# Kernel tuning notes

Measured on AMD Instinct MI355X. Metric: run time of the kernel, lower is better.

The kernel has to match this reference:

```python
import jax, jax.numpy as jnp
import numpy as np

N_NEURONS = 50000
N_BKG = 100
N_SYN_BASIS = 5
N_EDGES = 500000
BATCH = 1
SEQ_T = 250
BKG_RATE_PROB = 0.25  # bkg_firing_rate(250) * 0.001


def setup_inputs() -> dict:
    key = jax.random.key(0)
    k_w, k_tau, k_sp, k_r, k_c = jax.random.split(key, 5)
    weights = jax.random.normal(k_w, (N_EDGES,), dtype=jnp.float32)
    tau_syn = jax.random.uniform(k_tau, (N_EDGES, N_SYN_BASIS), dtype=jnp.float32)
    # Bernoulli background spikes, shape [B*T, n_bkg_units]
    spikes = (jax.random.uniform(k_sp, (BATCH * SEQ_T, N_BKG)) < BKG_RATE_PROB).astype(jnp.float32)
    rows = jax.random.randint(k_r, (N_EDGES,), 0, N_NEURONS, dtype=jnp.int32)
    cols = jax.random.randint(k_c, (N_EDGES,), 0, N_BKG, dtype=jnp.int32)
    return {"weights": weights, "tau_syn": tau_syn, "spikes": spikes,
            "rows": rows, "cols": cols}


def reference(weights, tau_syn, spikes, rows, cols):
    # Per-receptor edge values: weights[e] * tau_syn[e, r]  -> [E, R]
    vals = weights[:, None] * tau_syn
    # Densify the (identical-structure) sparse matrix once for all receptors;
    # duplicate (row, col) indices accumulate, matching tf.sparse semantics
    # used through sparse_dense_matmul. W: [N, K, R]
    W = jnp.zeros((N_NEURONS, N_BKG, N_SYN_BASIS), dtype=spikes.dtype).at[rows, cols].add(vals)
    # i_receptor[r] = sparse_w_in @ spikes.T -> stacked [R, N, BT];
    # tf.transpose reverses axes -> [BT, N, R]; fused here as one einsum.
    out = jnp.einsum('nkr,bk->bnr', W, spikes)  # [BT, N, R]
    return out.reshape(BATCH, SEQ_T, N_NEURONS * N_SYN_BASIS)
```

## Files before the change

kernel.cpp:

```cpp
#include <hip/hip_runtime.h>


#define N_NEURONS 50000
#define N_BKG     100
#define N_SYN     5
#define N_EDGES   500000
#define SEQ_T     250
#define NCOL      (N_NEURONS * N_SYN)
#define RPB       16
#define NBINS     (N_NEURONS / RPB)
#define NPART     8
#define CAP_P     64
#define RECS_BIN  (NPART * CAP_P)
#define CPADF     80
#define BCOLS     80
#define STRIDE_J  37

#define LDS_BYTES 32000

#define WS_COUNT_OFF 0
#define WS_SPB_OFF   131072
#define WS_REC_OFF   262144

typedef __attribute__((ext_vector_type(8))) short bf16x8;
typedef __attribute__((ext_vector_type(4))) float f32x4;

__device__ inline unsigned short bf16_rne(float f) {
    unsigned u = __builtin_bit_cast(unsigned, f);
    u += 0x7FFFu + ((u >> 16) & 1u);
    return (unsigned short)(u >> 16);
}
__device__ inline float bf16_up(unsigned hw) {
    return __builtin_bit_cast(float, hw << 16);
}

__global__ __launch_bounds__(256) void bucket_kernel(
        const float* __restrict__ weights,
        const float* __restrict__ tau,
        const int*   __restrict__ rows,
        const int*   __restrict__ cols,
        const float* __restrict__ spikes,
        unsigned* __restrict__ count,
        uint4* __restrict__ rec,
        bf16x8* __restrict__ spbf) {
    int gid = blockIdx.x * 256 + threadIdx.x;
    if (gid < 4096) {
        int lane = gid & 63;
        int kk   = (gid >> 6) & 3;
        int nt   = gid >> 8;
        int t    = nt * 16 + (lane & 15);
        int k0   = kk * 32 + (lane >> 4) * 8;
        bf16x8 v;
#pragma unroll
        for (int i = 0; i < 8; ++i) {
            float s = 0.f;
            if (t < SEQ_T && (k0 + i) < N_BKG)
                s = spikes[t * N_BKG + k0 + i];
            v[i] = (short)bf16_rne(s);
        }
        spbf[gid] = v;
    }
    if (gid >= N_EDGES) return;
    int row = rows[gid];
    int col = cols[gid];
    float w = weights[gid];
    const float* tp = tau + (size_t)gid * N_SYN;
    int bin  = row >> 4;
    int part = blockIdx.x & (NPART - 1);
    unsigned slot = atomicAdd(&count[part * NBINS + bin], 1u);
    if (slot >= CAP_P) return;
    uint4 r;
    r.x = ((unsigned)col << 4) | (unsigned)(row & 15);
    r.y = (unsigned)bf16_rne(w * tp[0]) | ((unsigned)bf16_rne(w * tp[1]) << 16);
    r.z = (unsigned)bf16_rne(w * tp[2]) | ((unsigned)bf16_rne(w * tp[3]) << 16);
    r.w = (unsigned)bf16_rne(w * tp[4]);
    rec[(size_t)bin * RECS_BIN + part * CAP_P + slot] = r;
}

__global__ __launch_bounds__(256, 4) void fused_kernel(
        const unsigned* __restrict__ count,
        const uint4* __restrict__ rec,
        const bf16x8* __restrict__ spbf,
        float* __restrict__ out) {
    __shared__ __align__(16) char lds[LDS_BYTES];
    float* slice = (float*)lds;

    const int tid = threadIdx.x;
    const int l   = tid & 63;
    const int wv  = tid >> 6;
    const int lc  = l & 15;
    const int lq  = l >> 4;

    const int orig = blockIdx.x;
    const int xcd  = orig & 7;
    const int j    = orig >> 3;
    const int qx   = (xcd < 5) ? 391 : 390;
    const int base = (xcd < 5) ? xcd * 391 : 5 * 391 + (xcd - 5) * 390;
    const int bin  = base + (j * STRIDE_J) % qx;

    const uint4* rbin = rec + (size_t)bin * RECS_BIN;
    unsigned cntA = count[wv * NBINS + bin];
    unsigned cntB = count[(4 + wv) * NBINS + bin];
    if (cntA > CAP_P) cntA = CAP_P;
    if (cntB > CAP_P) cntB = CAP_P;
    uint4 ra = rbin[wv * CAP_P + l];
    uint4 rb = rbin[(4 + wv) * CAP_P + l];
    bool havea = (unsigned)l < cntA;
    bool haveb = (unsigned)l < cntB;

    {
        f32x4* s4 = (f32x4*)lds;
        f32x4 z = (f32x4){0.f, 0.f, 0.f, 0.f};
#pragma unroll
        for (int jj = 0; jj < 8; ++jj) {
            int i = tid + jj * 256;
            if (i < 2000) s4[i] = z;
        }
    }
    __syncthreads();

    if (havea) {
        float* bp = &slice[(ra.x >> 4) * CPADF + (ra.x & 15u) * N_SYN];
        atomicAdd(bp + 0, bf16_up(ra.y & 0xFFFFu));
        atomicAdd(bp + 1, bf16_up(ra.y >> 16));
        atomicAdd(bp + 2, bf16_up(ra.z & 0xFFFFu));
        atomicAdd(bp + 3, bf16_up(ra.z >> 16));
        atomicAdd(bp + 4, bf16_up(ra.w & 0xFFFFu));
    }
    if (haveb) {
        float* bp = &slice[(rb.x >> 4) * CPADF + (rb.x & 15u) * N_SYN];
        atomicAdd(bp + 0, bf16_up(rb.y & 0xFFFFu));
        atomicAdd(bp + 1, bf16_up(rb.y >> 16));
        atomicAdd(bp + 2, bf16_up(rb.z & 0xFFFFu));
        atomicAdd(bp + 3, bf16_up(rb.z >> 16));
        atomicAdd(bp + 4, bf16_up(rb.w & 0xFFFFu));
    }
    __syncthreads();

    bf16x8 hi[5];
#pragma unroll
    for (int jj = 0; jj < 5; ++jj) {
        int m  = tid + jj * 256;
        int c  = m % BCOLS;
        int kb = m / BCOLS;
#pragma unroll
        for (int i = 0; i < 8; ++i) {
            int k = kb * 8 + i;
            float v = (k < N_BKG) ? slice[k * CPADF + c] : 0.f;
            hi[jj][i] = (short)bf16_rne(v);
        }
    }
    __syncthreads();
#pragma unroll
    for (int jj = 0; jj < 5; ++jj) {
        int m  = tid + jj * 256;
        int c  = m % BCOLS;
        int kb = m / BCOLS;
        unsigned bo = (unsigned)(((c << 8) + (kb << 4)) ^ ((c & 7) << 4));
        *(bf16x8*)(lds + bo) = hi[jj];
    }

    bf16x8 bs[4][4];
#pragma unroll
    for (int n = 0; n < 4; ++n)
#pragma unroll
        for (int kk = 0; kk < 4; ++kk)
            bs[n][kk] = spbf[((wv * 4 + n) * 4 + kk) * 64 + l];
    __syncthreads();

    const size_t cb = (size_t)bin * BCOLS;
#pragma unroll
    for (int m = 0; m < 5; ++m) {
        f32x4 acc[4];
#pragma unroll
        for (int n = 0; n < 4; ++n)
            acc[n] = (f32x4){0.f, 0.f, 0.f, 0.f};

        int c = m * 16 + lc;
#pragma unroll
        for (int kk = 0; kk < 4; ++kk) {
            int bor = (((c << 8) + (kk << 6) + (lq << 4)) ^ ((c & 7) << 4));
            bf16x8 ah = *(const bf16x8*)(lds + bor);
#pragma unroll
            for (int n = 0; n < 4; ++n)
                acc[n] = __builtin_amdgcn_mfma_f32_16x16x32_bf16(
                             ah, bs[n][kk], acc[n], 0, 0, 0);
        }
        size_t cs = cb + m * 16 + lq * 4;
#pragma unroll
        for (int n = 0; n < 4; ++n) {
            int t = (wv * 4 + n) * 16 + lc;
            if (t < SEQ_T)
                *(f32x4*)(out + (size_t)t * NCOL + cs) = acc[n];
        }
    }
}

extern "C" void kernel_launch(void* const* d_in, const int* in_sizes, int n_in,
                              void* d_out, int out_size, void* d_ws, size_t ws_size,
                              hipStream_t stream) {
    const float* weights = (const float*)d_in[0];
    const float* tau     = (const float*)d_in[1];
    const float* spikes  = (const float*)d_in[2];
    const int*   rows    = (const int*)d_in[3];
    const int*   cols    = (const int*)d_in[4];
    float* out = (float*)d_out;

    char* ws = (char*)d_ws;
    unsigned* count = (unsigned*)(ws + WS_COUNT_OFF);
    bf16x8*   spbf  = (bf16x8*)(ws + WS_SPB_OFF);
    uint4*    rec   = (uint4*)(ws + WS_REC_OFF);

    hipMemsetAsync(count, 0, NPART * NBINS * sizeof(unsigned), stream);

    int eblocks = (N_EDGES + 255) / 256;
    bucket_kernel<<<eblocks, 256, 0, stream>>>(weights, tau, rows, cols, spikes,
                                               count, rec, spbf);

    fused_kernel<<<NBINS, 256, 0, stream>>>(count, rec, spbf, out);
}
```

Baseline: 112.6 us.

## Split fused scatter+GEMM into separate scatter and streaming GEMM kernels

Replaces the single fused kernel with two. A scatter kernel densifies each bin into bf16 weights and writes them to workspace in MFMA-fragment order. A separate GEMM kernel then streams those fragments over a 2D grid, with each wave reusing its spike fragments across many M-tiles and writing output rows contiguously. This aims to decouple the atomic-heavy LDS scatter from the output-bandwidth-bound GEMM and to improve write locality, at the cost of an extra launch and a roundtrip of the dense bf16 weights (about 20 MB) through global memory.

Measured after the change: 146.4 us. +30.1%, slower.

```diff
diff --git a/kernel.cpp b/kernel.cpp
--- a/kernel.cpp
+++ b/kernel.cpp
@@ -13,14 +13,15 @@
 #define CAP_P     64
 #define RECS_BIN  (NPART * CAP_P)
 #define CPADF     80
-#define BCOLS     80
-#define STRIDE_J  37
+#define NMT       15625
+#define MT_BLK    63
 
 #define LDS_BYTES 32000
 
 #define WS_COUNT_OFF 0
 #define WS_SPB_OFF   131072
 #define WS_REC_OFF   262144
+#define WS_WG_OFF    25862144
 
 typedef __attribute__((ext_vector_type(8))) short bf16x8;
 typedef __attribute__((ext_vector_type(4))) float f32x4;
@@ -77,26 +78,16 @@
     rec[(size_t)bin * RECS_BIN + part * CAP_P + slot] = r;
 }
 
-__global__ __launch_bounds__(256, 4) void fused_kernel(
+__global__ __launch_bounds__(256, 4) void scatter_kernel(
         const unsigned* __restrict__ count,
         const uint4* __restrict__ rec,
-        const bf16x8* __restrict__ spbf,
-        float* __restrict__ out) {
-    __shared__ __align__(16) char lds[LDS_BYTES];
-    float* slice = (float*)lds;
+        bf16x8* __restrict__ wg) {
+    __shared__ __align__(16) float slice[N_BKG * CPADF];
 
     const int tid = threadIdx.x;
+    const int bin = blockIdx.x;
     const int l   = tid & 63;
     const int wv  = tid >> 6;
-    const int lc  = l & 15;
-    const int lq  = l >> 4;
-
-    const int orig = blockIdx.x;
-    const int xcd  = orig & 7;
-    const int j    = orig >> 3;
-    const int qx   = (xcd < 5) ? 391 : 390;
-    const int base = (xcd < 5) ? xcd * 391 : 5 * 391 + (xcd - 5) * 390;
-    const int bin  = base + (j * STRIDE_J) % qx;
 
     const uint4* rbin = rec + (size_t)bin * RECS_BIN;
     unsigned cntA = count[wv * NBINS + bin];
@@ -109,11 +100,11 @@
     bool haveb = (unsigned)l < cntB;
 
     {
-        f32x4* s4 = (f32x4*)lds;
+        f32x4* s4 = (f32x4*)slice;
         f32x4 z = (f32x4){0.f, 0.f, 0.f, 0.f};
 #pragma unroll
-        for (int jj = 0; jj < 8; ++jj) {
-            int i = tid + jj * 256;
+        for (int j = 0; j < 8; ++j) {
+            int i = tid + j * 256;
             if (i < 2000) s4[i] = z;
         }
     }
@@ -137,62 +128,62 @@
     }
     __syncthreads();
 
-    bf16x8 hi[5];
-#pragma unroll
-    for (int jj = 0; jj < 5; ++jj) {
-        int m  = tid + jj * 256;
-        int c  = m % BCOLS;
-        int kb = m / BCOLS;
+#pragma unroll
+    for (int j = 0; j < 5; ++j) {
+        int u  = tid + j * 256;
+        int c  = u % 80;
+        int kb = u / 80;
+        bf16x8 v;
 #pragma unroll
         for (int i = 0; i < 8; ++i) {
             int k = kb * 8 + i;
-            float v = (k < N_BKG) ? slice[k * CPADF + c] : 0.f;
-            hi[jj][i] = (short)bf16_rne(v);
+            float f = (k < N_BKG) ? slice[k * CPADF + c] : 0.f;
+            v[i] = (short)bf16_rne(f);
         }
-    }
-    __syncthreads();
-#pragma unroll
-    for (int jj = 0; jj < 5; ++jj) {
-        int m  = tid + jj * 256;
-        int c  = m % BCOLS;
-        int kb = m / BCOLS;
-        unsigned bo = (unsigned)(((c << 8) + (kb << 4)) ^ ((c & 7) << 4));
-        *(bf16x8*)(lds + bo) = hi[jj];
-    }
-
-    bf16x8 bs[4][4];
-#pragma unroll
-    for (int n = 0; n < 4; ++n)
-#pragma unroll
-        for (int kk = 0; kk < 4; ++kk)
-            bs[n][kk] = spbf[((wv * 4 + n) * 4 + kk) * 64 + l];
-    __syncthreads();
-
-    const size_t cb = (size_t)bin * BCOLS;
-#pragma unroll
-    for (int m = 0; m < 5; ++m) {
-        f32x4 acc[4];
-#pragma unroll
-        for (int n = 0; n < 4; ++n)
-            acc[n] = (f32x4){0.f, 0.f, 0.f, 0.f};
-
-        int c = m * 16 + lc;
-#pragma unroll
-        for (int kk = 0; kk < 4; ++kk) {
-            int bor = (((c << 8) + (kk << 6) + (lq << 4)) ^ ((c & 7) << 4));
-            bf16x8 ah = *(const bf16x8*)(lds + bor);
-#pragma unroll
-            for (int n = 0; n < 4; ++n)
-                acc[n] = __builtin_amdgcn_mfma_f32_16x16x32_bf16(
-                             ah, bs[n][kk], acc[n], 0, 0, 0);
-        }
-        size_t cs = cb + m * 16 + lq * 4;
-#pragma unroll
-        for (int n = 0; n < 4; ++n) {
-            int t = (wv * 4 + n) * 16 + lc;
-            if (t < SEQ_T)
-                *(f32x4*)(out + (size_t)t * NCOL + cs) = acc[n];
-        }
+        size_t idx = ((size_t)(bin * 5 + (c >> 4)) * 4 + (kb >> 2)) * 64
+                   + ((c & 15) | ((kb & 3) << 4));
+        wg[idx] = v;
+    }
+}
+
+__global__ __launch_bounds__(256, 4) void gemm_kernel(
+        const bf16x8* __restrict__ wg,
+        const bf16x8* __restrict__ spbf,
+        float* __restrict__ out) {
+    const int tid = threadIdx.x;
+    const int l   = tid & 63;
+    const int wv  = tid >> 6;
+    const int lc  = l & 15;
+    const int lq  = l >> 4;
+    const int cr  = blockIdx.x;
+    const int nt  = blockIdx.y * 4 + wv;
+    const int t   = nt * 16 + lc;
+    const int m0  = cr * MT_BLK;
+    const int mcnt = (cr < 248) ? MT_BLK : (NMT - 248 * MT_BLK);
+
+    bf16x8 bs[4];
+#pragma unroll
+    for (int kk = 0; kk < 4; ++kk)
+        bs[kk] = spbf[(nt * 4 + kk) * 64 + l];
+
+    const bf16x8* wp = wg + (size_t)m0 * 256 + l;
+    const bool tok = (t < SEQ_T);
+    float* orow = out + (size_t)t * NCOL + lq * 4;
+
+#pragma unroll 2
+    for (int m = 0; m < mcnt; ++m) {
+        f32x4 acc = (f32x4){0.f, 0.f, 0.f, 0.f};
+        bf16x8 ah0 = wp[0];
+        bf16x8 ah1 = wp[64];
+        bf16x8 ah2 = wp[128];
+        bf16x8 ah3 = wp[192];
+        acc = __builtin_amdgcn_mfma_f32_16x16x32_bf16(ah0, bs[0], acc, 0, 0, 0);
+        acc = __builtin_amdgcn_mfma_f32_16x16x32_bf16(ah1, bs[1], acc, 0, 0, 0);
+        acc = __builtin_amdgcn_mfma_f32_16x16x32_bf16(ah2, bs[2], acc, 0, 0, 0);
+        acc = __builtin_amdgcn_mfma_f32_16x16x32_bf16(ah3, bs[3], acc, 0, 0, 0);
+        wp += 256;
+        if (tok)
+            *(f32x4*)(orow + (size_t)(m0 + m) * 16) = acc;
     }
 }
 
@@ -210,6 +201,7 @@
     unsigned* count = (unsigned*)(ws + WS_COUNT_OFF);
     bf16x8*   spbf  = (bf16x8*)(ws + WS_SPB_OFF);
     uint4*    rec   = (uint4*)(ws + WS_REC_OFF);
+    bf16x8*   wg    = (bf16x8*)(ws + WS_WG_OFF);
 
     hipMemsetAsync(count, 0, NPART * NBINS * sizeof(unsigned), stream);
 
@@ -217,5 +209,7 @@
     bucket_kernel<<<eblocks, 256, 0, stream>>>(weights, tau, rows, cols, spikes,
                                                count, rec, spbf);
 
-    fused_kernel<<<NBINS, 256, 0, stream>>>(count, rec, spbf, out);
-}
+    scatter_kernel<<<NBINS, 256, 0, stream>>>(count, rec, wg);
+
+    gemm_kernel<<<dim3(249, 4), 256, 0, stream>>>(wg, spbf, out);
+}
```
